# Kernel optimization log

Hardware: AMD Instinct MI355X
Metric: run time of the kernel (lower is better)

## Reference

```python
import jax, jax.numpy as jnp
import numpy as np

EPS = 1e-08


def setup_inputs() -> dict:
    key = jax.random.key(0)
    B, C, T = 4, 512, 32000
    x = jax.random.normal(key, (B, C, T), dtype=jnp.float32)
    weight = jnp.ones((C,), dtype=jnp.float32)
    bias = jnp.zeros((C,), dtype=jnp.float32)
    return {"x": x, "weight": weight, "bias": bias}


def reference(x, weight, bias):
    # Cumulative LayerNorm over (C, 0..t) for each time step t, 3D input (B, C, T).
    # Note: sum_C(cumsum_T(x)) == cumsum_T(sum_C(x)); reduce channels first (cheaper, same math).
    B, C, T = x.shape
    step = jnp.arange(1, T + 1, dtype=x.dtype)            # (T,)
    count = (step * C)[None, None, :]                     # (1,1,T)
    cum_sum = jnp.cumsum(x.sum(axis=1, keepdims=True), axis=-1)          # (B,1,T)
    cum_sum_sq = jnp.cumsum((x * x).sum(axis=1, keepdims=True), axis=-1)  # (B,1,T)
    cum_mean = cum_sum / count
    cum_var = jnp.maximum(cum_sum_sq / count - cum_mean * cum_mean, 0.0)
    y = (x - cum_mean) / jnp.sqrt(cum_var + EPS)
    return y * weight[None, :, None] + bias[None, :, None]
```

## Files before the change

kernel.cpp:

```cpp
#include <hip/hip_runtime.h>
#include <math.h>

#define EPS 1e-8

constexpr int W = 32;
constexpr int W4 = W / 4;
constexpr int NTHR = 256;
constexpr int CMAX = 512;

__global__ __launch_bounds__(NTHR, 4) void clnorm_reduce(
    const float4* __restrict__ x4, double* __restrict__ scanS,
    double* __restrict__ scanQ, double* __restrict__ aggS,
    double* __restrict__ aggQ, int B, int C, int T, int nCh) {
  const int T4 = T >> 2;
  const int ch = blockIdx.x;
  const int b = blockIdx.y;
  const int tid = threadIdx.x;
  const int t0 = ch * W;
  const int t40 = t0 >> 2;

  const int p = tid >> 3;
  const int t4 = tid & (W4 - 1);
  const int cPer = C / 32;

  float4 s4 = make_float4(0.f, 0.f, 0.f, 0.f);
  float4 q4 = make_float4(0.f, 0.f, 0.f, 0.f);
  if (t40 + t4 < T4) {
    const float4* xp = x4 + ((size_t)b * C + (size_t)p * cPer) * T4 + t40 + t4;
#pragma unroll 4
    for (int k = 0; k < cPer; ++k) {
      float4 v = xp[(size_t)k * T4];
      s4.x += v.x;
      s4.y += v.y;
      s4.z += v.z;
      s4.w += v.w;
      q4.x = fmaf(v.x, v.x, q4.x);
      q4.y = fmaf(v.y, v.y, q4.y);
      q4.z = fmaf(v.z, v.z, q4.z);
      q4.w = fmaf(v.w, v.w, q4.w);
    }
  }
  __shared__ float4 ps4[32 * W4];
  __shared__ float4 pq4[32 * W4];
  ps4[p * W4 + t4] = s4;
  pq4[p * W4 + t4] = q4;
  __syncthreads();

  const int wave = tid >> 6;
  const int lane = tid & 63;
  if (wave < 2 && lane < W) {
    const float* src = (wave == 0) ? (const float*)ps4 : (const float*)pq4;
    double a = 0.0;
#pragma unroll 8
    for (int pp = 0; pp < 32; ++pp)
      a += (double)src[pp * W + lane];
    for (int off = 1; off < W; off <<= 1) {
      double v = __shfl_up(a, off, 64);
      if (lane >= off) a += v;
    }
    if (t0 + lane < T) {
      double* dst = (wave == 0) ? scanS : scanQ;
      dst[(size_t)b * T + t0 + lane] = a;
    }
    if (lane == W - 1) {
      double* ad = (wave == 0) ? aggS : aggQ;
      ad[(size_t)b * nCh + ch] = a;
    }
  }
}

__global__ __launch_bounds__(512) void clnorm_scanagg(
    const double* __restrict__ aggS, const double* __restrict__ aggQ,
    double* __restrict__ offS, double* __restrict__ offQ, int nCh) {
  const int b = blockIdx.x;
  const int tid = threadIdx.x;
  __shared__ double shS[512];
  __shared__ double shQ[512];

  const int i0 = tid * 2, i1 = tid * 2 + 1;
  const size_t base = (size_t)b * nCh;
  double s0 = (i0 < nCh) ? aggS[base + i0] : 0.0;
  double s1 = (i1 < nCh) ? aggS[base + i1] : 0.0;
  double q0 = (i0 < nCh) ? aggQ[base + i0] : 0.0;
  double q1 = (i1 < nCh) ? aggQ[base + i1] : 0.0;
  shS[tid] = s0 + s1;
  shQ[tid] = q0 + q1;
  __syncthreads();
  for (int off = 1; off < 512; off <<= 1) {
    double vs = (tid >= off) ? shS[tid - off] : 0.0;
    double vq = (tid >= off) ? shQ[tid - off] : 0.0;
    __syncthreads();
    shS[tid] += vs;
    shQ[tid] += vq;
    __syncthreads();
  }
  double exS = shS[tid] - (s0 + s1);
  double exQ = shQ[tid] - (q0 + q1);
  if (i0 < nCh) {
    offS[base + i0] = exS;
    offQ[base + i0] = exQ;
  }
  if (i1 < nCh) {
    offS[base + i1] = exS + s0;
    offQ[base + i1] = exQ + q0;
  }
}

__global__ __launch_bounds__(NTHR, 4) void clnorm_apply(
    const float4* __restrict__ x4, const float* __restrict__ wgt,
    const float* __restrict__ bias, const double* __restrict__ scanS,
    const double* __restrict__ scanQ, const double* __restrict__ offS,
    const double* __restrict__ offQ, float4* __restrict__ y4, int B, int C,
    int T, int nCh) {
  const int T4 = T >> 2;
  const int ch = blockIdx.x;
  const int b = blockIdx.y;
  const int tid = threadIdx.x;
  const int t0 = ch * W;
  const int t40 = t0 >> 2;

  __shared__ float w_sh[CMAX];
  __shared__ float b_sh[CMAX];
  __shared__ __align__(16) float m_sh[W];
  __shared__ __align__(16) float r_sh[W];

  for (int c = tid; c < C; c += NTHR) {
    w_sh[c] = wgt[c];
    b_sh[c] = bias[c];
  }

  if (tid < W && t0 + tid < T) {
    double s = offS[(size_t)b * nCh + ch] + scanS[(size_t)b * T + t0 + tid];
    double q = offQ[(size_t)b * nCh + ch] + scanQ[(size_t)b * T + t0 + tid];
    double cnt = (double)(t0 + tid + 1) * (double)C;
    double m = s / cnt;
    double var = q / cnt - m * m;
    if (var < 0.0) var = 0.0;
    m_sh[tid] = (float)m;
    r_sh[tid] = (float)(1.0 / sqrt(var + EPS));
  }
  __syncthreads();

  const int c0 = tid >> 3;
  const int t4 = tid & (W4 - 1);
  if (t40 + t4 >= T4) return;
  const float4 mv = *(const float4*)&m_sh[t4 * 4];
  const float4 rv = *(const float4*)&r_sh[t4 * 4];
  const float4* xp = x4 + ((size_t)b * C + c0) * T4 + t40 + t4;
  float4* yp = y4 + ((size_t)b * C + c0) * T4 + t40 + t4;
#pragma unroll 4
  for (int j = 0; j < CMAX / 32; ++j) {
    int c = c0 + j * 32;
    float4 xv = xp[(size_t)(j * 32) * T4];
    float wc = w_sh[c], bc = b_sh[c];
    float4 yv;
    yv.x = (xv.x - mv.x) * rv.x * wc + bc;
    yv.y = (xv.y - mv.y) * rv.y * wc + bc;
    yv.z = (xv.z - mv.z) * rv.z * wc + bc;
    yv.w = (xv.w - mv.w) * rv.w * wc + bc;
    yp[(size_t)(j * 32) * T4] = yv;
  }
}

extern "C" void kernel_launch(void* const* d_in, const int* in_sizes, int n_in,
                              void* d_out, int out_size, void* d_ws,
                              size_t ws_size, hipStream_t stream) {
  const float4* x4 = (const float4*)d_in[0];
  const float* w = (const float*)d_in[1];
  const float* bias = (const float*)d_in[2];
  float4* y4 = (float4*)d_out;

  int B = 4;
  int C = in_sizes[1];
  int T = in_sizes[0] / (B * C);
  int nCh = (T + W - 1) / W;

  double* scanS = (double*)d_ws;
  double* scanQ = scanS + (size_t)B * T;
  double* aggS = scanQ + (size_t)B * T;
  double* aggQ = aggS + (size_t)B * nCh;
  double* offS = aggQ + (size_t)B * nCh;
  double* offQ = offS + (size_t)B * nCh;

  dim3 g(nCh, B);
  clnorm_reduce<<<g, NTHR, 0, stream>>>(x4, scanS, scanQ, aggS, aggQ, B, C, T,
                                        nCh);
  clnorm_scanagg<<<dim3(B), 512, 0, stream>>>(aggS, aggQ, offS, offQ, nCh);
  clnorm_apply<<<g, NTHR, 0, stream>>>(x4, w, bias, scanS, scanQ, offS, offQ,
                                       y4, B, C, T, nCh);
}
```

Before: 512.8 us.

## Widen time tiles to 128 and reverse apply block order with nontemporal I/O

```diff
diff --git a/kernel.cpp b/kernel.cpp
--- a/kernel.cpp
+++ b/kernel.cpp
@@ -3,10 +3,13 @@
 
 #define EPS 1e-8
 
-constexpr int W = 32;
+constexpr int W = 128;
 constexpr int W4 = W / 4;
 constexpr int NTHR = 256;
+constexpr int RG = 8;
 constexpr int CMAX = 512;
+
+typedef float vf4 __attribute__((ext_vector_type(4)));
 
 __global__ __launch_bounds__(NTHR, 4) void clnorm_reduce(
     const float4* __restrict__ x4, double* __restrict__ scanS,
@@ -19,17 +22,17 @@
   const int t0 = ch * W;
   const int t40 = t0 >> 2;
 
-  const int p = tid >> 3;
+  const int rg = tid >> 5;
   const int t4 = tid & (W4 - 1);
-  const int cPer = C / 32;
+  const int rowsPer = C / RG;
 
   float4 s4 = make_float4(0.f, 0.f, 0.f, 0.f);
   float4 q4 = make_float4(0.f, 0.f, 0.f, 0.f);
   if (t40 + t4 < T4) {
-    const float4* xp = x4 + ((size_t)b * C + (size_t)p * cPer) * T4 + t40 + t4;
-#pragma unroll 4
-    for (int k = 0; k < cPer; ++k) {
-      float4 v = xp[(size_t)k * T4];
+    const float4* xp = x4 + ((size_t)b * C + rg) * T4 + t40 + t4;
+#pragma unroll 8
+    for (int k = 0; k < rowsPer; ++k) {
+      float4 v = xp[(size_t)k * RG * T4];
       s4.x += v.x;
       s4.y += v.y;
       s4.z += v.z;
@@ -40,69 +43,73 @@
       q4.w = fmaf(v.w, v.w, q4.w);
     }
   }
-  __shared__ float4 ps4[32 * W4];
-  __shared__ float4 pq4[32 * W4];
-  ps4[p * W4 + t4] = s4;
-  pq4[p * W4 + t4] = q4;
+  __shared__ float4 ps4[RG * W4];
+  __shared__ float4 pq4[RG * W4];
+  ps4[rg * W4 + t4] = s4;
+  pq4[rg * W4 + t4] = q4;
   __syncthreads();
 
   const int wave = tid >> 6;
   const int lane = tid & 63;
-  if (wave < 2 && lane < W) {
+  if (wave < 2) {
     const float* src = (wave == 0) ? (const float*)ps4 : (const float*)pq4;
-    double a = 0.0;
-#pragma unroll 8
-    for (int pp = 0; pp < 32; ++pp)
-      a += (double)src[pp * W + lane];
-    for (int off = 1; off < W; off <<= 1) {
-      double v = __shfl_up(a, off, 64);
-      if (lane >= off) a += v;
+    const int ta = lane * 2;
+    double a0 = 0.0, a1 = 0.0;
+#pragma unroll
+    for (int p = 0; p < RG; ++p) {
+      a0 += (double)src[p * W + ta];
+      a1 += (double)src[p * W + ta + 1];
     }
-    if (t0 + lane < T) {
-      double* dst = (wave == 0) ? scanS : scanQ;
-      dst[(size_t)b * T + t0 + lane] = a;
+    const double pair = a0 + a1;
+    double incl = pair;
+    for (int off = 1; off < 64; off <<= 1) {
+      double v = __shfl_up(incl, off, 64);
+      if (lane >= off) incl += v;
     }
-    if (lane == W - 1) {
+    const double excl = incl - pair;
+    double* dst = (wave == 0) ? scanS : scanQ;
+    if (t0 + ta < T) {
+      dst[(size_t)b * T + t0 + ta] = excl + a0;
+      dst[(size_t)b * T + t0 + ta + 1] = excl + pair;
+    }
+    if (lane == 63) {
       double* ad = (wave == 0) ? aggS : aggQ;
-      ad[(size_t)b * nCh + ch] = a;
+      ad[(size_t)b * nCh + ch] = incl;
     }
   }
 }
 
-__global__ __launch_bounds__(512) void clnorm_scanagg(
+__global__ __launch_bounds__(256) void clnorm_scanagg(
     const double* __restrict__ aggS, const double* __restrict__ aggQ,
     double* __restrict__ offS, double* __restrict__ offQ, int nCh) {
   const int b = blockIdx.x;
   const int tid = threadIdx.x;
-  __shared__ double shS[512];
-  __shared__ double shQ[512];
-
-  const int i0 = tid * 2, i1 = tid * 2 + 1;
+  __shared__ double shS[256];
+  __shared__ double shQ[256];
   const size_t base = (size_t)b * nCh;
-  double s0 = (i0 < nCh) ? aggS[base + i0] : 0.0;
-  double s1 = (i1 < nCh) ? aggS[base + i1] : 0.0;
-  double q0 = (i0 < nCh) ? aggQ[base + i0] : 0.0;
-  double q1 = (i1 < nCh) ? aggQ[base + i1] : 0.0;
-  shS[tid] = s0 + s1;
-  shQ[tid] = q0 + q1;
-  __syncthreads();
-  for (int off = 1; off < 512; off <<= 1) {
-    double vs = (tid >= off) ? shS[tid - off] : 0.0;
-    double vq = (tid >= off) ? shQ[tid - off] : 0.0;
+  double carS = 0.0, carQ = 0.0;
+  for (int r0 = 0; r0 < nCh; r0 += 256) {
+    const int i = r0 + tid;
+    double s = (i < nCh) ? aggS[base + i] : 0.0;
+    double q = (i < nCh) ? aggQ[base + i] : 0.0;
+    shS[tid] = s;
+    shQ[tid] = q;
     __syncthreads();
-    shS[tid] += vs;
-    shQ[tid] += vq;
+    for (int off = 1; off < 256; off <<= 1) {
+      double vs = (tid >= off) ? shS[tid - off] : 0.0;
+      double vq = (tid >= off) ? shQ[tid - off] : 0.0;
+      __syncthreads();
+      shS[tid] += vs;
+      shQ[tid] += vq;
+      __syncthreads();
+    }
+    if (i < nCh) {
+      offS[base + i] = carS + shS[tid] - s;
+      offQ[base + i] = carQ + shQ[tid] - q;
+    }
+    carS += shS[255];
+    carQ += shQ[255];
     __syncthreads();
-  }
-  double exS = shS[tid] - (s0 + s1);
-  double exQ = shQ[tid] - (q0 + q1);
-  if (i0 < nCh) {
-    offS[base + i0] = exS;
-    offQ[base + i0] = exQ;
-  }
-  if (i1 < nCh) {
-    offS[base + i1] = exS + s0;
-    offQ[base + i1] = exQ + q0;
   }
 }
 
@@ -113,8 +120,8 @@
     const double* __restrict__ offQ, float4* __restrict__ y4, int B, int C,
     int T, int nCh) {
   const int T4 = T >> 2;
-  const int ch = blockIdx.x;
-  const int b = blockIdx.y;
+  const int ch = nCh - 1 - blockIdx.x;
+  const int b = B - 1 - blockIdx.y;
   const int tid = threadIdx.x;
   const int t0 = ch * W;
   const int t40 = t0 >> 2;
@@ -128,7 +135,6 @@
     w_sh[c] = wgt[c];
     b_sh[c] = bias[c];
   }
-
   if (tid < W && t0 + tid < T) {
     double s = offS[(size_t)b * nCh + ch] + scanS[(size_t)b * T + t0 + tid];
     double q = offQ[(size_t)b * nCh + ch] + scanQ[(size_t)b * T + t0 + tid];
@@ -141,24 +147,26 @@
   }
   __syncthreads();
 
-  const int c0 = tid >> 3;
+  const int rg = tid >> 5;
   const int t4 = tid & (W4 - 1);
   if (t40 + t4 >= T4) return;
-  const float4 mv = *(const float4*)&m_sh[t4 * 4];
-  const float4 rv = *(const float4*)&r_sh[t4 * 4];
-  const float4* xp = x4 + ((size_t)b * C + c0) * T4 + t40 + t4;
-  float4* yp = y4 + ((size_t)b * C + c0) * T4 + t40 + t4;
-#pragma unroll 4
-  for (int j = 0; j < CMAX / 32; ++j) {
-    int c = c0 + j * 32;
-    float4 xv = xp[(size_t)(j * 32) * T4];
-    float wc = w_sh[c], bc = b_sh[c];
-    float4 yv;
+  const float4 mv = ((const float4*)m_sh)[t4];
+  const float4 rv = ((const float4*)r_sh)[t4];
+  const vf4* xp =
+      (const vf4*)(x4 + ((size_t)b * C + rg) * T4 + t40 + t4);
+  vf4* yp = (vf4*)(y4 + ((size_t)b * C + rg) * T4 + t40 + t4);
+  const int rowsPer = C / RG;
+#pragma unroll 8
+  for (int k = 0; k < rowsPer; ++k) {
+    const int c = rg + k * RG;
+    vf4 xv = __builtin_nontemporal_load(xp + (size_t)k * RG * T4);
+    const float wc = w_sh[c], bc = b_sh[c];
+    vf4 yv;
     yv.x = (xv.x - mv.x) * rv.x * wc + bc;
     yv.y = (xv.y - mv.y) * rv.y * wc + bc;
     yv.z = (xv.z - mv.z) * rv.z * wc + bc;
     yv.w = (xv.w - mv.w) * rv.w * wc + bc;
-    yp[(size_t)(j * 32) * T4] = yv;
+    __builtin_nontemporal_store(yv, yp + (size_t)k * RG * T4);
   }
 }
 
@@ -185,7 +193,7 @@
   dim3 g(nCh, B);
   clnorm_reduce<<<g, NTHR, 0, stream>>>(x4, scanS, scanQ, aggS, aggQ, B, C, T,
                                         nCh);
-  clnorm_scanagg<<<dim3(B), 512, 0, stream>>>(aggS, aggQ, offS, offQ, nCh);
+  clnorm_scanagg<<<dim3(B), 256, 0, stream>>>(aggS, aggQ, offS, offQ, nCh);
   clnorm_apply<<<g, NTHR, 0, stream>>>(x4, w, bias, scanS, scanQ, offS, offQ,
                                        y4, B, C, T, nCh);
 }
```

After: 470.9 us. 1.09x faster.
